# Optimization experiments

Hardware: AMD Instinct MI355X
Metric: run time of the kernel (lower is better)

The kernel has to match this reference:

```python
import jax, jax.numpy as jnp
import numpy as np

N = 50000          # site nodes
L = 32             # max URL token length
E = 64             # embed_size
H = 128            # hidden_size
E_SIM = 800000     # edges per relation in blocks
E_SUB = 200000     # 'sim' edges classified at the end
NEG = 0.01         # LeakyReLU negative slope

def leaky(x):
    return jnp.where(x >= 0, x, NEG * x)

def lstm_final(x, mask, Wih, Whh, b, reverse):
    # x: [N, L, E], mask: [N, L] bool. Returns packed-sequence final hidden [N, E].
    if reverse:
        x = x[:, ::-1, :]
        mask = mask[:, ::-1]
    h0 = jnp.zeros((x.shape[0], Whh.shape[1]), x.dtype)
    def step(carry, inp):
        h, c = carry
        xt, mt = inp
        g = xt @ Wih.T + h @ Whh.T + b
        i, f, gg, o = jnp.split(g, 4, axis=-1)  # PyTorch gate order i,f,g,o
        cn = jax.nn.sigmoid(f) * c + jax.nn.sigmoid(i) * jnp.tanh(gg)
        hn = jax.nn.sigmoid(o) * jnp.tanh(cn)
        m = mt[:, None]
        return (jnp.where(m, hn, h), jnp.where(m, cn, c)), None
    (h, _), _ = jax.lax.scan(step, (h0, h0), (x.transpose(1, 0, 2), mask.T))
    return h

def graph_conv(h, src, dst, W, b):
    # DGL GraphConv, norm='both': D_dst^{-1/2} A D_src^{-1/2} h W + b  (degrees clamped to >=1)
    n = h.shape[0]
    ones = jnp.ones(src.shape[0], h.dtype)
    out_deg = jnp.clip(jax.ops.segment_sum(ones, src, num_segments=n), 1.0)
    in_deg = jnp.clip(jax.ops.segment_sum(ones, dst, num_segments=n), 1.0)
    feat = h * jax.lax.rsqrt(out_deg)[:, None]
    if W.shape[0] > W.shape[1]:
        feat = feat @ W  # project before gather/scatter when in_dim > out_dim (as DGL does)
        rst = jax.ops.segment_sum(feat[src], dst, num_segments=n)
    else:
        rst = jax.ops.segment_sum(feat[src], dst, num_segments=n) @ W
    return rst * jax.lax.rsqrt(in_deg)[:, None] + b

def setup_inputs():
    key = jax.random.key(0)
    ks = iter(jax.random.split(key, 64))
    def nrm(shape, scale=0.05):
        return jax.random.normal(next(ks), shape, dtype=jnp.float32) * scale
    inp = {}
    inp["inputs_s"] = jax.random.randint(next(ks), (N, L), 0, 128)
    lengths = jax.random.randint(next(ks), (N,), 1, L + 1)
    inp["inputs_sm"] = (jnp.arange(L)[None, :] < lengths[:, None]).astype(jnp.int32)
    inp["inputs_c"] = jax.random.randint(next(ks), (N, 1), 0, 101)
    inp["inputs_co"] = jax.random.randint(next(ks), (N, 1), 0, 92)
    inp["inputs_sl"] = jax.random.randint(next(ks), (N, 1), 0, 6)
    for name, m in [("sim_src", E_SIM), ("sim_dst", E_SIM), ("user_src", E_SIM),
                    ("user_dst", E_SIM), ("esub_src", E_SUB), ("esub_dst", E_SUB)]:
        inp[name] = jax.random.randint(next(ks), (m,), 0, N)
    inp["emb_url"] = nrm((128, E)); inp["emb_cat"] = nrm((101, E))
    inp["emb_country"] = nrm((92, E)); inp["emb_sl"] = nrm((6, E))
    for d in ("f", "b"):
        inp["Wih_" + d] = nrm((4 * E, E)); inp["Whh_" + d] = nrm((4 * E, E))
        inp["b_" + d] = nrm((4 * E,))  # b_ih + b_hh folded into one bias
    inp["fc_W"] = nrm((E, 2 * E)); inp["fc_b"] = nrm((E,))
    for i, din in enumerate([4 * E, H]):
        for rel in ("sim", "user"):
            inp["gcn%d_%s_W" % (i, rel)] = nrm((din, H))
            inp["gcn%d_%s_b" % (i, rel)] = nrm((H,))
    inp["cls_W1"] = nrm((H, 2 * H)); inp["cls_b1"] = nrm((H,))
    inp["bn_g"] = jnp.ones((H,), jnp.float32); inp["bn_b"] = jnp.zeros((H,), jnp.float32)
    inp["cls_W2"] = nrm((2, H)); inp["cls_b2"] = nrm((2,))
    return inp

def reference(inputs_s, inputs_sm, inputs_c, inputs_co, inputs_sl,
              sim_src, sim_dst, user_src, user_dst, esub_src, esub_dst,
              emb_url, emb_cat, emb_country, emb_sl,
              Wih_f, Whh_f, b_f, Wih_b, Whh_b, b_b, fc_W, fc_b,
              gcn0_sim_W, gcn0_sim_b, gcn0_user_W, gcn0_user_b,
              gcn1_sim_W, gcn1_sim_b, gcn1_user_W, gcn1_user_b,
              cls_W1, cls_b1, bn_g, bn_b, cls_W2, cls_b2):
    mask = inputs_sm.astype(bool)
    x = emb_url[inputs_s]                                # [N, L, E]
    hf = lstm_final(x, mask, Wih_f, Whh_f, b_f, False)   # h_n[0]
    hb = lstm_final(x, mask, Wih_b, Whh_b, b_b, True)    # h_n[1]
    h_url = leaky(jnp.concatenate([hf, hb], -1) @ fc_W.T + fc_b)  # dropout = identity (eval)
    h = jnp.concatenate([h_url, emb_cat[inputs_c[:, 0]],
                         emb_country[inputs_co[:, 0]], emb_sl[inputs_sl[:, 0]]], -1)  # [N, 4E]
    layers = [(gcn0_sim_W, gcn0_sim_b, gcn0_user_W, gcn0_user_b),
              (gcn1_sim_W, gcn1_sim_b, gcn1_user_W, gcn1_user_b)]
    for Ws, bs, Wu, bu in layers:  # HeteroGraphConv aggregate='sum'
        h = leaky(graph_conv(h, sim_src, sim_dst, Ws, bs)
                  + graph_conv(h, user_src, user_dst, Wu, bu))
    feat = jnp.concatenate([h[esub_src], h[esub_dst]], -1)  # [E_SUB, 2H]
    z = feat @ cls_W1.T + cls_b1
    z = (z - z.mean(0)) * jax.lax.rsqrt(z.var(0) + 1e-5) * bn_g + bn_b  # BatchNorm1d (batch stats)
    z = jnp.maximum(z, 0.0)
    return z @ cls_W2.T + cls_b2
```

## Files before the change

kernel.cpp:

```cpp
#include <hip/hip_runtime.h>
#include <hip/hip_bf16.h>
#include <stdint.h>

#define N_NODES 50000
#define SEQ_L   32
#define NE_BIG  800000
#define NE_SUB  200000
#define DSTRIDE 64
#define BNREP   64

typedef __hip_bfloat16 bf16;
typedef unsigned short u16;
typedef unsigned int u32;
typedef _Float16 f16;
typedef _Float16 v8h __attribute__((ext_vector_type(8)));
typedef float v4f __attribute__((ext_vector_type(4)));

#if __has_builtin(__builtin_amdgcn_exp2f)
#define EXP2(x) __builtin_amdgcn_exp2f(x)
#else
extern "C" __device__ float __ocml_native_exp2_f32(float);
#define EXP2(x) __ocml_native_exp2_f32(x)
#endif
#define LOG2E  1.4426950408889634f
#define LOG2E2 2.8853900817779268f
#define GCLAMP 43.280851226668902f

__device__ __forceinline__ float b2f(bf16 x) { return __bfloat162float(x); }
__device__ __forceinline__ float leakyf(float v) { return v >= 0.f ? v : 0.01f * v; }
__device__ __forceinline__ u16 f2h_bits(float x) { f16 h = (f16)x; u16 b; __builtin_memcpy(&b, &h, 2); return b; }
__device__ __forceinline__ float h2f(u16 b) { f16 h; __builtin_memcpy(&h, &b, 2); return (float)h; }
__device__ __forceinline__ uint pack2h(float a, float b) { return (uint)f2h_bits(a) | ((uint)f2h_bits(b) << 16); }

__device__ __forceinline__ float ldf(const void* p, int i, int isbf) {
  return isbf ? b2f(((const bf16*)p)[i]) : ((const float*)p)[i];
}

__device__ __forceinline__ int detect_isbf(const u16* __restrict__ u) {
  __shared__ int insane;
  if (threadIdx.x == 0) insane = 0;
  __syncthreads();
  int expo = (u[threadIdx.x * 2] >> 7) & 0xFF;
  if (expo >= 147) atomicAdd(&insane, 1);
  __syncthreads();
  return insane == 0;
}

#define NBUCK   391
#define BSHIFT  7
#define BCAP    3072
#define P1_EPT   32
#define P1_CHUNK (256 * P1_EPT)
#define P1_NCH   ((NE_BIG + P1_CHUNK - 1) / P1_CHUNK)
#define P1_BLOCKS (P1_NCH * 2)

struct PrepArgs {
  const void* Whh_f; const void* Whh_b; const void* fc_W; const void* cls_W1;
  const void* g0sW; const void* g0uW; const void* g1sW; const void* g1uW;
  const void* emb_cat; const void* emb_country; const void* emb_sl;
  const void* fc_b; const void* cls_b1; const void* g0sb; const void* g0ub;
  const void* g1sb; const void* g1ub; const void* bn_g; const void* bn_b;
  const void* cls_W2; const void* cls_b2;
  const void* emb_url; const void* Wih_f; const void* b_f; const void* Wih_b; const void* b_b;
  f16* Whh_h; u16* Bfc; u16* BW1; u16* Bg0; u16* Bg1;
  u16* embc_h; u16* embco_h; u16* embs_h;
  float* fcb; float* b1; float* g0sbP; float* g0ubP; float* g1sbP; float* g1ubP;
  float* bngP; float* bnbP; float* W2P; float* b2P;
  int* dflag;
  float* Xperm;
  const int* sm; int* lens; int* cnt33;
  const int* s0; const int* d0; const int* s1; const int* d1;
  int* cnt4; int* gcur; u32* bucket;
};

__global__ __launch_bounds__(256) void prep_graph_kernel(PrepArgs A) {
  const int bid = blockIdx.x;
  const int t = threadIdx.x;

  __shared__ u32 stage[P1_CHUNK];
  __shared__ int hcnt[NBUCK];
  __shared__ int hstart[NBUCK];
  __shared__ int gbase[NBUCK];
  __shared__ int scanbuf[512];

  if (bid < P1_BLOCKS) {
    const int rel = bid & 1;
    const int chunk = bid >> 1;
    const int* s = rel ? A.s1 : A.s0;
    const int* d = rel ? A.d1 : A.d0;
    int* outdeg = A.cnt4 + (size_t)rel * 2 * N_NODES;
    int* gcur = A.gcur + rel * NBUCK;
    u32* bbuf = A.bucket + (size_t)rel * NBUCK * BCAP;
    const int e0 = chunk * P1_CHUNK;
    const int cn = min(NE_BIG - e0, P1_CHUNK);

    for (int b = t; b < NBUCK; b += 256) hcnt[b] = 0;
    __syncthreads();
#pragma unroll
    for (int k = 0; k < P1_EPT; ++k) {
      int i = t + k * 256;
      if (i < cn) {
        int sv = s[e0 + i], dv = d[e0 + i];
        atomicAdd(&outdeg[sv], 1);
        atomicAdd(&hcnt[dv >> BSHIFT], 1);
      }
    }
    __syncthreads();
    scanbuf[t] = (t < NBUCK) ? hcnt[t] : 0;
    scanbuf[t + 256] = (t + 256 < NBUCK) ? hcnt[t + 256] : 0;
    __syncthreads();
    for (int off = 1; off < 512; off <<= 1) {
      int a0 = (t >= off) ? scanbuf[t - off] : 0;
      int a1 = (t + 256 >= off) ? scanbuf[t + 256 - off] : 0;
      __syncthreads();
      scanbuf[t] += a0;
      scanbuf[t + 256] += a1;
      __syncthreads();
    }
    for (int b = t; b < NBUCK; b += 256) {
      int c = hcnt[b];
      int st = scanbuf[b] - c;
      hstart[b] = st;
      gbase[b] = (c > 0) ? atomicAdd(&gcur[b], c) : 0;
      scanbuf[b] = st;
    }
    __syncthreads();
#pragma unroll
    for (int k = 0; k < P1_EPT; ++k) {
      int i = t + k * 256;
      if (i < cn) {
        int sv = s[e0 + i], dv = d[e0 + i];
        int b = dv >> BSHIFT;
        int pos = atomicAdd(&scanbuf[b], 1);
        stage[pos] = ((u32)b << 23) | ((u32)sv << 7) | (u32)(dv & 127);
      }
    }
    __syncthreads();
    for (int i = t; i < cn; i += 256) {
      u32 r = stage[i];
      int b = r >> 23;
      int o = gbase[b] + (i - hstart[b]);
      if (o < BCAP) bbuf[(size_t)b * BCAP + o] = r;
    }
    return;
  }

  const int b = bid - P1_BLOCKS;

  if (b >= 990) {
    int i = (b - 990) * 256 + t;
    if (i >= N_NODES) return;
    int len = 0;
#pragma unroll
    for (int tt = 0; tt < SEQ_L; ++tt) len += __builtin_nontemporal_load(A.sm + i * SEQ_L + tt);
    A.lens[i] = len;
    atomicAdd(&A.cnt33[len], 1);
    return;
  }

  const int isbf = detect_isbf((const u16*)A.emb_url);
  auto cpy = [&](const void* s, float* d, int n, int boff) {
    int i = (b - boff) * 256 + t;
    if (i < n) d[i] = ldf(s, i, isbf);
  };
  auto cvh = [&](const void* s, u16* d, int n, int boff) {
    int i = (b - boff) * 256 + t;
    if (i < n) d[i] = f2h_bits(ldf(s, i, isbf));
  };
  auto cvhW = [&](const void* s, u16* d, int boff) {
    int i = (b - boff) * 256 + t;
    float sc = ((i >> 12) == 2) ? LOG2E2 : LOG2E;
    d[i] = f2h_bits(ldf(s, i, isbf) * sc);
  };
  auto trh = [&](const void* s, u16* d, int R, int C, int KOFF, int boff) {
    int i = (b - boff) * 256 + t;
    if (i < R * C) { int r = i / C, c = i % C; d[c * 256 + KOFF + r] = f2h_bits(ldf(s, i, isbf)); }
  };
  if      (b <   64) cvhW(A.Whh_f, (u16*)A.Whh_h, 0);
  else if (b <  128) cvhW(A.Whh_b, (u16*)(A.Whh_h + 16384), 64);
  else if (b <  160) cvh(A.fc_W, A.Bfc, 8192, 128);
  else if (b <  288) cvh(A.cls_W1, A.BW1, 32768, 160);
  else if (b <  416) trh(A.g0sW, A.Bg0, 256, 128, 0, 288);
  else if (b <  544) trh(A.g0uW, A.Bg0 + 128 * 256, 256, 128, 0, 416);
  else if (b <  608) trh(A.g1sW, A.Bg1, 128, 128, 0, 544);
  else if (b <  672) trh(A.g1uW, A.Bg1, 128, 128, 128, 608);
  else if (b <  698) cvh(A.emb_cat, A.embc_h, 6464, 672);
  else if (b <  721) cvh(A.emb_country, A.embco_h, 5888, 698);
  else if (b <  723) cvh(A.emb_sl, A.embs_h, 384, 721);
  else if (b <  724) cpy(A.fc_b, A.fcb, 64, 723);
  else if (b <  725) cpy(A.cls_b1, A.b1, 128, 724);
  else if (b <  726) cpy(A.g0sb, A.g0sbP, 128, 725);
  else if (b <  727) cpy(A.g0ub, A.g0ubP, 128, 726);
  else if (b <  728) cpy(A.g1sb, A.g1sbP, 128, 727);
  else if (b <  729) cpy(A.g1ub, A.g1ubP, 128, 728);
  else if (b <  730) cpy(A.bn_g, A.bngP, 128, 729);
  else if (b <  731) cpy(A.bn_b, A.bnbP, 128, 730);
  else if (b <  732) cpy(A.cls_W2, A.W2P, 256, 731);
  else if (b <  733) { cpy(A.cls_b2, A.b2P, 2, 732); if (t == 0) A.dflag[0] = isbf; }
  else if (b <  989) {
    int bb = b - 733;
    int dir = bb >> 7;
    int v = bb & 127;
    const void* Wih = dir ? A.Wih_b : A.Wih_f;
    const void* bias = dir ? A.b_b : A.b_f;
    __shared__ float embL[64];
    if (t < 64) embL[t] = ldf(A.emb_url, v * 64 + t, isbf);
    __syncthreads();
    float acc = ldf(bias, t, isbf);
#pragma unroll 8
    for (int j = 0; j < 64; ++j) acc += embL[j] * ldf(Wih, t * 64 + j, isbf);
    int g = t >> 6, unit = t & 63;
    float sc = (g == 2) ? LOG2E2 : LOG2E;
    A.Xperm[(size_t)dir * 128 * 256 + v * 256 + unit * 4 + g] = acc * sc;
  }
}
#define PG_BLOCKS (P1_BLOCKS + 1186)

__global__ __launch_bounds__(256) void permfill_rsq_kernel(
    const int* __restrict__ lens, const int* __restrict__ cnt33, int* __restrict__ cur33,
    int* __restrict__ perm,
    int* __restrict__ cnt4, float* __restrict__ rsq4,
    const u32* __restrict__ bucket, const int* __restrict__ gcur,
    u16* __restrict__ col0, u16* __restrict__ col1)
{
  const int b = blockIdx.x, t = threadIdx.x;
  __shared__ u16 colL[128 * DSTRIDE];
  __shared__ int curL[128];

  if (b < 196) {
    int i = b * 256 + t;
    if (i >= N_NODES) return;
    int len = lens[i];
    int base = 0;
    for (int l = len + 1; l <= SEQ_L; ++l) base += cnt33[l];
    int p = atomicAdd(&cur33[len], 1);
    perm[base + p] = i;
  } else if (b < 196 + 2 * NBUCK) {
    int k = b - 196;
    int rel = k / NBUCK;
    int bk = k % NBUCK;
    const u32* bb = bucket + ((size_t)rel * NBUCK + bk) * BCAP;
    u16* col = rel ? col1 : col0;
    int cnt = gcur[rel * NBUCK + bk];
    if (cnt > BCAP) cnt = BCAP;
    if (t < 128) curL[t] = 0;
    __syncthreads();
    for (int i = t; i < cnt; i += 256) {
      u32 r = bb[i];
      int dl = r & 127;
      int sv = (r >> 7) & 0xFFFF;
      int p = atomicAdd(&curL[dl], 1);
      if (p < DSTRIDE) colL[dl * DSTRIDE + p] = (u16)sv;
    }
    __syncthreads();
    const int node0 = bk << BSHIFT;
    for (int idx = t; idx < 128 * (DSTRIDE / 2); idx += 256) {
      int row = idx >> 5;
      int node = node0 + row;
      if (node < N_NODES)
        ((uint*)(col + (size_t)node * DSTRIDE))[idx & 31] = ((const uint*)colL)[idx];
    }
    if (t < 128) {
      int node = node0 + t;
      if (node < N_NODES) {
        int c = curL[t];
        cnt4[rel * 2 * N_NODES + N_NODES + node] = c;
        float cc = (c < 1) ? 1.f : (float)c;
        rsq4[rel * 2 * N_NODES + N_NODES + node] = __builtin_amdgcn_rsqf(cc);
      }
    }
  } else {
    int idx = (b - 196 - 2 * NBUCK) * 256 + t;
    int i;
    if (idx < N_NODES) i = idx;
    else if (idx < 2 * N_NODES) i = idx + N_NODES;
    else return;
    int c = cnt4[i]; if (c < 1) c = 1;
    rsq4[i] = __builtin_amdgcn_rsqf((float)c);
  }
}
#define PR_BLOCKS (196 + 2 * NBUCK + 391)

__global__ __launch_bounds__(256, 4) void lstm_mfma_kernel(
    const int* __restrict__ perm, const int* __restrict__ lens,
    const int* __restrict__ toksg,
    const float* __restrict__ Xperm,
    const f16* __restrict__ Whh_h,
    u16* __restrict__ hcat_h,
    int nnodes)
{
  __shared__ __align__(16) f16 H[2][64 * 72];
  __shared__ int permL[64];
  __shared__ int lensL[64];
  __shared__ int cutL[SEQ_L + 1];
  const int tid = threadIdx.x;
  const int w = tid >> 6;
  const int lane = tid & 63;
  const int quad = lane >> 4;
  const int lid = lane & 15;
  const int dir = blockIdx.y;
  char* Hc = (char*)&H[0][0];

  if (tid < 64) {
    int gid = blockIdx.x * 64 + tid;
    int node = -1, len = 0;
    if (gid < nnodes) { node = perm[gid]; len = lens[node]; }
    permL[tid] = node; lensL[tid] = len;
  }
  {
    uint* Hz = (uint*)Hc;
    for (int i = tid; i < 2 * 64 * 72 / 2; i += 256) Hz[i] = 0u;
  }
  __syncthreads();
  if (tid <= SEQ_L) {
    int c = 0;
#pragma unroll 8
    for (int n = 0; n < 64; ++n) c += (lensL[n] > tid) ? 1 : 0;
    cutL[tid] = c;
  }
  for (int idx = tid; idx < 64 * SEQ_L; idx += 256) {
    int node = idx >> 5, tp = idx & 31;
    int len = lensL[node];
    if (tp < len) {
      int s = dir ? (len - 1 - tp) : tp;
      int i = s * 64 + node;
      Hc[(i >> 4) * 144 + 128 + (i & 15)] = (char)toksg[(size_t)permL[node] * SEQ_L + tp];
    }
  }
  __syncthreads();
  const int tmax = lensL[0];

  const f16* Wd = Whh_h + (size_t)dir * 256 * 64;
  v8h Bf[4][2];
#pragma unroll
  for (int g = 0; g < 4; ++g)
#pragma unroll
    for (int kf = 0; kf < 2; ++kf)
      Bf[g][kf] = *(const v8h*)(Wd + (g * 64 + w * 16 + lid) * 64 + kf * 32 + quad * 8);

  float creg[16];
  f16 hreg[16];
#pragma unroll
  for (int i = 0; i < 16; ++i) { creg[i] = 0.f; hreg[i] = (f16)0.f; }

  const char* Xp = (const char*)(Xperm + (size_t)dir * 128 * 256);
  const uint xlane = (uint)((w * 16 + lid) * 16);

  for (int step = 0; step < tmax; ++step) {
    const int rb = step & 1, wb = rb ^ 1;
    const int cut = cutL[step];
#pragma unroll
    for (int mt = 0; mt < 4; ++mt) {
      uint tok4 = *(const uint*)(Hc + (step * 4 + mt) * 144 + 128 + quad * 4);
      float4 xr[4];
#pragma unroll
      for (int r = 0; r < 4; ++r) {
        uint tok = (tok4 >> (8 * r)) & 255u;
        xr[r] = *(const float4*)(Xp + (tok << 10) + xlane);
      }
      const f16* hb = &H[rb][0];
      int arow = (mt * 16 + lid) * 72 + quad * 8;
      v8h a0 = *(const v8h*)(hb + arow);
      v8h a1 = *(const v8h*)(hb + arow + 32);
      v4f acc[4];
      acc[0] = (v4f){xr[0].x, xr[1].x, xr[2].x, xr[3].x};
      acc[1] = (v4f){xr[0].y, xr[1].y, xr[2].y, xr[3].y};
      acc[2] = (v4f){xr[0].z, xr[1].z, xr[2].z, xr[3].z};
      acc[3] = (v4f){xr[0].w, xr[1].w, xr[2].w, xr[3].w};
#pragma unroll
      for (int g = 0; g < 4; ++g) {
        acc[g] = __builtin_amdgcn_mfma_f32_16x16x32_f16(a0, Bf[g][0], acc[g], 0, 0, 0);
        acc[g] = __builtin_amdgcn_mfma_f32_16x16x32_f16(a1, Bf[g][1], acc[g], 0, 0, 0);
      }
#pragma unroll
      for (int r = 0; r < 4; ++r) {
        int idx = mt * 4 + r;
        int nd = mt * 16 + quad * 4 + r;
        bool act = nd < cut;
        float gi = acc[0][r];
        float gf = acc[1][r];
        float gG = acc[2][r];
        float go = acc[3][r];
        float A = EXP2(-gi);
        float B = EXP2(-gf);
        float C = EXP2(-go);
        float D = EXP2(fminf(gG, GCLAMP));
        float sf = __builtin_amdgcn_rcpf(1.f + B);
        float sitg = (D - 1.f) * __builtin_amdgcn_rcpf((1.f + A) * (D + 1.f));
        float cn = sf * creg[idx] + sitg;
        float E = EXP2(fminf(cn * LOG2E2, GCLAMP));
        float hn = (E - 1.f) * __builtin_amdgcn_rcpf((1.f + C) * (E + 1.f));
        if (act) { creg[idx] = cn; hreg[idx] = (f16)hn; }
        H[wb][nd * 72 + w * 16 + lid] = hreg[idx];
      }
    }
    __syncthreads();
  }
#pragma unroll
  for (int mt = 0; mt < 4; ++mt)
#pragma unroll
    for (int r = 0; r < 4; ++r) {
      int nd = mt * 16 + quad * 4 + r;
      int gnode = permL[nd];
      if (gnode >= 0) {
        u16 bits; f16 hv = hreg[mt * 4 + r]; __builtin_memcpy(&bits, &hv, 2);
        hcat_h[(size_t)gnode * 128 + dir * 64 + w * 16 + lid] = bits;
      }
    }
}

template<int K, int COLS, int AMODE, bool LEAKY, int OHS, bool EMB, bool BNS>
__global__ __launch_bounds__(256) void mfma_gemm(
    const u16* __restrict__ Ah,
    const int* __restrict__ esrc, const int* __restrict__ edst, const u16* __restrict__ Fh,
    const u16* __restrict__ B,
    const float* __restrict__ bias, const float* __restrict__ bias2,
    const float* __restrict__ rs0, const float* __restrict__ rs1,
    u16* __restrict__ outh0, u16* __restrict__ outh1,
    const int* __restrict__ ic, const int* __restrict__ ico, const int* __restrict__ isl,
    const u16* __restrict__ ech, const u16* __restrict__ ecoh, const u16* __restrict__ eslh,
    float* __restrict__ bnsums,
    int nrows)
{
  constexpr int AST = K + 8;
  constexpr int ABYTES = 64 * AST * 2;
  constexpr int EBYTES = 64 * 129 * 4;
  constexpr int SBYTES = (ABYTES > EBYTES) ? ABYTES : EBYTES;
  __shared__ __align__(16) char smem[SBYTES];
  u16* As = (u16*)smem;
  float* Es = (float*)smem;
  __shared__ int idxL[128];
  __shared__ float bnred[BNS ? 512 : 1];

  const int tid = threadIdx.x;
  const int w = tid >> 6;
  const int lane = tid & 63;
  const int quad = lane >> 4;
  const int lid = lane & 15;
  const int r0 = blockIdx.x * 64;

  if (AMODE == 2) {
    if (tid < 64) {
      int row = r0 + tid;
      idxL[tid] = (row < nrows) ? esrc[row] : -1;
      idxL[64 + tid] = (row < nrows) ? edst[row] : -1;
    }
    __syncthreads();
    for (int idx = tid; idx < 64 * (K / 8); idx += 256) {
      int rn = idx / (K / 8), seg = idx % (K / 8);
      int half = seg >> 4, k8 = seg & 15;
      int base = idxL[half * 64 + rn];
      uint4 v = {0u, 0u, 0u, 0u};
      if (base >= 0) v = *(const uint4*)(Fh + (size_t)base * 128 + k8 * 8);
      *(uint4*)(As + rn * AST + seg * 8) = v;
    }
  } else {
    for (int idx = tid; idx < 64 * (K / 8); idx += 256) {
      int rn = idx / (K / 8), c8 = idx % (K / 8);
      int row = r0 + rn;
      uint4 v = {0u, 0u, 0u, 0u};
      if (row < nrows) v = *(const uint4*)(Ah + (size_t)row * K + c8 * 8);
      *(uint4*)(As + rn * AST + c8 * 8) = v;
    }
  }
  __syncthreads();

  constexpr int NT = COLS / 16;
  v4f acc[NT];
#pragma unroll
  for (int i = 0; i < NT; ++i) acc[i] = (v4f){0.f, 0.f, 0.f, 0.f};

  for (int kb = 0; kb < K / 32; ++kb) {
    v8h a = *(const v8h*)((const f16*)As + (w * 16 + lid) * AST + kb * 32 + quad * 8);
#pragma unroll
    for (int ct = 0; ct < NT; ++ct) {
      v8h b = *(const v8h*)((const f16*)B + (size_t)(ct * 16 + lid) * K + kb * 32 + quad * 8);
      acc[ct] = __builtin_amdgcn_mfma_f32_16x16x32_f16(a, b, acc[ct], 0, 0, 0);
    }
  }

  constexpr int NH = (COLS > 128) ? 2 : 1;
  constexpr int CH = COLS / NH;
  float bs = 0.f, bs2 = 0.f;
#pragma unroll
  for (int h = 0; h < NH; ++h) {
    __syncthreads();
#pragma unroll
    for (int ct = 0; ct < CH / 16; ++ct) {
      int ctg = h * (CH / 16) + ct;
#pragma unroll
      for (int r = 0; r < 4; ++r)
        Es[(w * 16 + quad * 4 + r) * 129 + ct * 16 + lid] = acc[ctg][r];
    }
    __syncthreads();
    for (int idx = tid; idx < 64 * CH; idx += 256) {
      int rn = idx / CH, c = idx % CH;
      int row = r0 + rn;
      float v = 0.f;
      if (row < nrows) {
        v = Es[rn * 129 + c];
        if (bias) v += bias[h * CH + c];
        if (bias2) v += bias2[h * CH + c];
        if (LEAKY) v = leakyf(v);
        const float* rs = (h == 0) ? rs0 : rs1;
        if (rs) v *= rs[row];
        u16* oh = (h == 0) ? outh0 : outh1;
        oh[(size_t)row * OHS + c] = f2h_bits(v);
      }
      if (BNS) { bs += v; bs2 += v * v; }
    }
  }
  if (BNS) {
    bnred[tid] = bs;
    bnred[256 + tid] = bs2;
    __syncthreads();
    if (tid < 128) {
      float* bnp = bnsums + (size_t)(blockIdx.x & (BNREP - 1)) * 256;
      atomicAdd(&bnp[tid], bnred[tid] + bnred[tid + 128]);
      atomicAdd(&bnp[128 + tid], bnred[256 + tid] + bnred[384 + tid]);
    }
  }
  if (EMB) {
    for (int idx = tid; idx < 64 * 192; idx += 256) {
      int rn = idx / 192, j = idx % 192;
      int row = r0 + rn;
      if (row >= nrows) continue;
      u16 v;
      if (j < 64)       v = ech [ic [row] * 64 + j];
      else if (j < 128) v = ecoh[ico[row] * 64 + (j - 64)];
      else              v = eslh[isl[row] * 64 + (j - 128)];
      outh0[(size_t)row * OHS + 64 + j] = v;
    }
  }
}

__global__ __launch_bounds__(256) void gather_merge0_kernel(
    const u16* __restrict__ colS, const int* __restrict__ cntS, const u16* __restrict__ Ps,
    const u16* __restrict__ colU, const int* __restrict__ cntU, const u16* __restrict__ Pu,
    const float* __restrict__ rsS, const float* __restrict__ rsU,
    const float* __restrict__ bS, const float* __restrict__ bU,
    u16* __restrict__ outh, int nnodes)
{
  int wave = threadIdx.x >> 6;
  int lane = threadIdx.x & 63;
  int node = __builtin_amdgcn_readfirstlane(blockIdx.x * 4 + wave);
  if (node >= nnodes) return;
  const uint* PS2 = (const uint*)Ps;
  const uint* PU2 = (const uint*)Pu;
  float2 aS = make_float2(0.f, 0.f), aU = make_float2(0.f, 0.f);
  {
    const u16* col = colS + (size_t)node * DSTRIDE;
    int cnt = min(cntS[node], DSTRIDE);
    int e = 0;
    for (; e + 4 <= cnt; e += 4) {
      uint v0 = PS2[(size_t)col[e] * 64 + lane];
      uint v1 = PS2[(size_t)col[e + 1] * 64 + lane];
      uint v2 = PS2[(size_t)col[e + 2] * 64 + lane];
      uint v3 = PS2[(size_t)col[e + 3] * 64 + lane];
      aS.x += h2f((u16)v0) + h2f((u16)v1) + h2f((u16)v2) + h2f((u16)v3);
      aS.y += h2f((u16)(v0 >> 16)) + h2f((u16)(v1 >> 16)) + h2f((u16)(v2 >> 16)) + h2f((u16)(v3 >> 16));
    }
    for (; e < cnt; ++e) {
      uint v = PS2[(size_t)col[e] * 64 + lane];
      aS.x += h2f((u16)v); aS.y += h2f((u16)(v >> 16));
    }
  }
  {
    const u16* col = colU + (size_t)node * DSTRIDE;
    int cnt = min(cntU[node], DSTRIDE);
    int e = 0;
    for (; e + 4 <= cnt; e += 4) {
      uint v0 = PU2[(size_t)col[e] * 64 + lane];
      uint v1 = PU2[(size_t)col[e + 1] * 64 + lane];
      uint v2 = PU2[(size_t)col[e + 2] * 64 + lane];
      uint v3 = PU2[(size_t)col[e + 3] * 64 + lane];
      aU.x += h2f((u16)v0) + h2f((u16)v1) + h2f((u16)v2) + h2f((u16)v3);
      aU.y += h2f((u16)(v0 >> 16)) + h2f((u16)(v1 >> 16)) + h2f((u16)(v2 >> 16)) + h2f((u16)(v3 >> 16));
    }
    for (; e < cnt; ++e) {
      uint v = PU2[(size_t)col[e] * 64 + lane];
      aU.x += h2f((u16)v); aU.y += h2f((u16)(v >> 16));
    }
  }
  float rS = rsS[node], rU = rsU[node];
  float2 bsv = ((const float2*)bS)[lane];
  float2 buv = ((const float2*)bU)[lane];
  float o0 = leakyf(aS.x * rS + bsv.x + aU.x * rU + buv.x);
  float o1 = leakyf(aS.y * rS + bsv.y + aU.y * rU + buv.y);
  ((uint*)outh)[(size_t)node * 64 + lane] = pack2h(o0, o1);
}

__global__ __launch_bounds__(256) void gather_cat1_kernel(
    const u16* __restrict__ colS, const int* __restrict__ cntS,
    const u16* __restrict__ colU, const int* __restrict__ cntU,
    const u16* __restrict__ Fh,
    const float* __restrict__ rsoutS, const float* __restrict__ rsoutU,
    const float* __restrict__ rsinS, const float* __restrict__ rsinU,
    u16* __restrict__ Acat, int nnodes)
{
  int wave = threadIdx.x >> 6;
  int lane = threadIdx.x & 63;
  int node = __builtin_amdgcn_readfirstlane(blockIdx.x * 4 + wave);
  if (node >= nnodes) return;
  const uint* F2 = (const uint*)Fh;
  float2 aS = make_float2(0.f, 0.f), aU = make_float2(0.f, 0.f);
  {
    const u16* col = colS + (size_t)node * DSTRIDE;
    int cnt = min(cntS[node], DSTRIDE);
    int e = 0;
    for (; e + 2 <= cnt; e += 2) {
      int s0 = col[e], s1 = col[e + 1];
      float c0 = rsoutS[s0], c1 = rsoutS[s1];
      uint v0 = F2[(size_t)s0 * 64 + lane];
      uint v1 = F2[(size_t)s1 * 64 + lane];
      aS.x += c0 * h2f((u16)v0) + c1 * h2f((u16)v1);
      aS.y += c0 * h2f((u16)(v0 >> 16)) + c1 * h2f((u16)(v1 >> 16));
    }
    for (; e < cnt; ++e) {
      int s = col[e]; float c = rsoutS[s];
      uint v = F2[(size_t)s * 64 + lane];
      aS.x += c * h2f((u16)v); aS.y += c * h2f((u16)(v >> 16));
    }
  }
  {
    const u16* col = colU + (size_t)node * DSTRIDE;
    int cnt = min(cntU[node], DSTRIDE);
    int e = 0;
    for (; e + 2 <= cnt; e += 2) {
      int s0 = col[e], s1 = col[e + 1];
      float c0 = rsoutU[s0], c1 = rsoutU[s1];
      uint v0 = F2[(size_t)s0 * 64 + lane];
      uint v1 = F2[(size_t)s1 * 64 + lane];
      aU.x += c0 * h2f((u16)v0) + c1 * h2f((u16)v1);
      aU.y += c0 * h2f((u16)(v0 >> 16)) + c1 * h2f((u16)(v1 >> 16));
    }
    for (; e < cnt; ++e) {
      int s = col[e]; float c = rsoutU[s];
      uint v = F2[(size_t)s * 64 + lane];
      aU.x += c * h2f((u16)v); aU.y += c * h2f((u16)(v >> 16));
    }
  }
  float rs = rsinS[node], ru = rsinU[node];
  ((uint*)Acat)[(size_t)node * 128 + lane] = pack2h(aS.x * rs, aS.y * rs);
  ((uint*)Acat)[(size_t)node * 128 + 64 + lane] = pack2h(aU.x * ru, aU.y * ru);
}

__global__ __launch_bounds__(256) void out_kernel(
    const u16* __restrict__ zh, const float* __restrict__ bnsums,
    const float* __restrict__ g, const float* __restrict__ bb, float M,
    const float* __restrict__ W2, const float* __restrict__ b2,
    void* __restrict__ out, int Mi, const int* __restrict__ flag)
{
  __shared__ float lds[128 * 65];
  __shared__ float red[64 * 8];
  __shared__ float ssL[256];
  const int tid = threadIdx.x;
  const int n = tid & 63;
  const int q = __builtin_amdgcn_readfirstlane(tid >> 6);
  const int r0 = blockIdx.x * 64;
  if (tid < 128) {
    float s = 0.f, s2 = 0.f;
#pragma unroll 8
    for (int r = 0; r < BNREP; ++r) {
      s  += bnsums[r * 256 + tid];
      s2 += bnsums[r * 256 + 128 + tid];
    }
    float mean = s / M;
    float var = s2 / M - mean * mean;
    float sc = g[tid] * __builtin_amdgcn_rsqf(var + 1e-5f);
    ssL[tid] = sc;
    ssL[128 + tid] = bb[tid] - mean * sc;
  }
  for (int idx = tid; idx < 64 * 128; idx += 256) {
    int rn = idx >> 7, j = idx & 127;
    int row = r0 + rn;
    lds[j * 65 + rn] = (row < Mi) ? h2f(zh[(size_t)row * 128 + j]) : 0.f;
  }
  __syncthreads();
  float a0 = 0.f, a1 = 0.f;
#pragma unroll 8
  for (int jj = 0; jj < 32; ++jj) {
    int j = q * 32 + jj;
    float y = lds[j * 65 + n] * ssL[j] + ssL[128 + j];
    y = y > 0.f ? y : 0.f;
    a0 += y * W2[j];
    a1 += y * W2[128 + j];
  }
  red[n * 8 + q * 2 + 0] = a0;
  red[n * 8 + q * 2 + 1] = a1;
  __syncthreads();
  if (q == 0 && (r0 + n) < Mi) {
    float o0 = red[n * 8] + red[n * 8 + 2] + red[n * 8 + 4] + red[n * 8 + 6] + b2[0];
    float o1 = red[n * 8 + 1] + red[n * 8 + 3] + red[n * 8 + 5] + red[n * 8 + 7] + b2[1];
    size_t oi = (size_t)(r0 + n) * 2;
    if (*flag) {
      ((bf16*)out)[oi + 0] = __float2bfloat16(o0);
      ((bf16*)out)[oi + 1] = __float2bfloat16(o1);
    } else {
      ((float*)out)[oi + 0] = o0;
      ((float*)out)[oi + 1] = o1;
    }
  }
}

extern "C" void kernel_launch(void* const* d_in, const int* in_sizes, int n_in,
                              void* d_out, int out_size, void* d_ws, size_t ws_size,
                              hipStream_t stream) {
  (void)in_sizes; (void)n_in; (void)out_size; (void)ws_size;
  const int N = N_NODES;
  const int* inputs_s  = (const int*)d_in[0];
  const int* inputs_sm = (const int*)d_in[1];
  const int* inputs_c  = (const int*)d_in[2];
  const int* inputs_co = (const int*)d_in[3];
  const int* inputs_sl = (const int*)d_in[4];
  const int* sim_src   = (const int*)d_in[5];
  const int* sim_dst   = (const int*)d_in[6];
  const int* user_src  = (const int*)d_in[7];
  const int* user_dst  = (const int*)d_in[8];
  const int* esub_src  = (const int*)d_in[9];
  const int* esub_dst  = (const int*)d_in[10];

  char* base = (char*)d_ws;
  size_t off = 0;
  auto alloc = [&](size_t bytes) -> char* {
    char* p = base + off;
    off += (bytes + 255) & ~(size_t)255;
    return p;
  };
  int* dflag    = (int*)alloc(256);
  f16* Whh_h    = (f16*)alloc(2 * 256 * 64 * 2);
  float* Xperm  = (float*)alloc(2 * 128 * 256 * 4);
  u16* Bfc      = (u16*)alloc(64 * 128 * 2);
  u16* BW1      = (u16*)alloc(128 * 256 * 2);
  u16* Bg0      = (u16*)alloc(256 * 256 * 2);
  u16* Bg1      = (u16*)alloc(128 * 256 * 2);
  u16* P_embc_h = (u16*)alloc(6464 * 2);
  u16* P_embco_h= (u16*)alloc(5888 * 2);
  u16* P_embs_h = (u16*)alloc(384 * 2);
  float* P_fcb  = (float*)alloc(64 * 4);
  float* P_b1   = (float*)alloc(128 * 4);
  float* P_g0sb = (float*)alloc(128 * 4);
  float* P_g0ub = (float*)alloc(128 * 4);
  float* P_g1sb = (float*)alloc(128 * 4);
  float* P_g1ub = (float*)alloc(128 * 4);
  float* P_bng  = (float*)alloc(128 * 4);
  float* P_bnb  = (float*)alloc(128 * 4);
  float* P_W2   = (float*)alloc(256 * 4);
  float* P_b2   = (float*)alloc(2 * 4);
  int* lens     = (int*)alloc((size_t)N * 4);
  int* perm     = (int*)alloc((size_t)N * 4);
  float* rsq4   = (float*)alloc((size_t)4 * N * 4);
  char* zbase   = alloc((size_t)4 * N * 4 + 4096 + BNREP * 256 * 4);
  int* cnt4     = (int*)zbase;
  int* cnt33    = (int*)(zbase + (size_t)4 * N * 4);
  int* cur33    = cnt33 + 64;
  int* gcur     = (int*)(zbase + (size_t)4 * N * 4 + 512);
  float* bnsums = (float*)(zbase + (size_t)4 * N * 4 + 4096);
  const size_t zbytes = (size_t)4 * N * 4 + 4096 + BNREP * 256 * 4;
  char* bufA = alloc((size_t)N * 256 * 4);
  char* bufB = alloc((size_t)N * 256 * 2);
  char* bufC = alloc((size_t)N * 256 * 2);
  char* bufE = alloc((size_t)N * 128 * 2);
  u16* h_h     = (u16*)bufA;
  u16* zh      = (u16*)bufA;
  u16* col_sim = (u16*)(bufA + (size_t)N * 256 * 2);
  u16* col_usr = (u16*)(bufA + (size_t)N * 256 * 2 + (size_t)N * DSTRIDE * 2);
  u16* hcat_h = (u16*)bufB;
  u16* h1_h   = (u16*)bufB;
  u32* bucket = (u32*)bufC;
  u16* Ps_h   = (u16*)bufC;
  u16* Pu_h   = Ps_h + (size_t)N * 128;
  u16* Acat   = (u16*)bufC;
  u16* F_h    = (u16*)bufE;

  const int NB64 = (N + 63) / 64;
  const int NBZ  = (NE_SUB + 63) / 64;

  hipMemsetAsync(zbase, 0, zbytes, stream);

  PrepArgs PA;
  PA.Whh_f = d_in[16]; PA.Whh_b = d_in[19]; PA.fc_W = d_in[21]; PA.cls_W1 = d_in[31];
  PA.g0sW = d_in[23]; PA.g0uW = d_in[25]; PA.g1sW = d_in[27]; PA.g1uW = d_in[29];
  PA.emb_cat = d_in[12]; PA.emb_country = d_in[13]; PA.emb_sl = d_in[14];
  PA.fc_b = d_in[22]; PA.cls_b1 = d_in[32]; PA.g0sb = d_in[24]; PA.g0ub = d_in[26];
  PA.g1sb = d_in[28]; PA.g1ub = d_in[30]; PA.bn_g = d_in[33]; PA.bn_b = d_in[34];
  PA.cls_W2 = d_in[35]; PA.cls_b2 = d_in[36];
  PA.emb_url = d_in[11]; PA.Wih_f = d_in[15]; PA.b_f = d_in[17]; PA.Wih_b = d_in[18]; PA.b_b = d_in[20];
  PA.Whh_h = Whh_h; PA.Bfc = Bfc; PA.BW1 = BW1; PA.Bg0 = Bg0; PA.Bg1 = Bg1;
  PA.embc_h = P_embc_h; PA.embco_h = P_embco_h; PA.embs_h = P_embs_h;
  PA.fcb = P_fcb; PA.b1 = P_b1; PA.g0sbP = P_g0sb; PA.g0ubP = P_g0ub; PA.g1sbP = P_g1sb; PA.g1ubP = P_g1ub;
  PA.bngP = P_bng; PA.bnbP = P_bnb; PA.W2P = P_W2; PA.b2P = P_b2;
  PA.dflag = dflag; PA.Xperm = Xperm;
  PA.sm = inputs_sm; PA.lens = lens; PA.cnt33 = cnt33;
  PA.s0 = sim_src; PA.d0 = sim_dst; PA.s1 = user_src; PA.d1 = user_dst;
  PA.cnt4 = cnt4; PA.gcur = gcur; PA.bucket = bucket;
  prep_graph_kernel<<<PG_BLOCKS, 256, 0, stream>>>(PA);

  permfill_rsq_kernel<<<PR_BLOCKS, 256, 0, stream>>>(lens, cnt33, cur33, perm, cnt4, rsq4,
                                                     bucket, gcur, col_sim, col_usr);

  lstm_mfma_kernel<<<dim3(NB64, 2), 256, 0, stream>>>(perm, lens, inputs_s, Xperm, Whh_h, hcat_h, N);

  mfma_gemm<128, 64, 1, true, 256, true, false><<<NB64, 256, 0, stream>>>(
      hcat_h, nullptr, nullptr, nullptr, Bfc, P_fcb, nullptr, nullptr, nullptr,
      h_h, nullptr, inputs_c, inputs_co, inputs_sl, P_embc_h, P_embco_h, P_embs_h, nullptr, N);

  mfma_gemm<256, 256, 1, false, 128, false, false><<<NB64, 256, 0, stream>>>(
      h_h, nullptr, nullptr, nullptr, Bg0, nullptr, nullptr, rsq4, rsq4 + 2 * N,
      Ps_h, Pu_h, nullptr, nullptr, nullptr, nullptr, nullptr, nullptr, nullptr, N);

  gather_merge0_kernel<<<(N + 3) / 4, 256, 0, stream>>>(col_sim, cnt4 + N, Ps_h,
                                                        col_usr, cnt4 + 3 * N, Pu_h,
                                                        rsq4 + N, rsq4 + 3 * N, P_g0sb, P_g0ub, h1_h, N);

  gather_cat1_kernel<<<(N + 3) / 4, 256, 0, stream>>>(col_sim, cnt4 + N, col_usr, cnt4 + 3 * N, h1_h,
                                                      rsq4, rsq4 + 2 * N, rsq4 + N, rsq4 + 3 * N, Acat, N);

  mfma_gemm<256, 128, 1, true, 128, false, false><<<NB64, 256, 0, stream>>>(
      Acat, nullptr, nullptr, nullptr, Bg1, P_g1sb, P_g1ub, nullptr, nullptr,
      F_h, nullptr, nullptr, nullptr, nullptr, nullptr, nullptr, nullptr, nullptr, N);

  mfma_gemm<256, 128, 2, false, 128, false, true><<<NBZ, 256, 0, stream>>>(
      nullptr, esub_src, esub_dst, F_h, BW1, P_b1, nullptr, nullptr, nullptr,
      zh, nullptr, nullptr, nullptr, nullptr, nullptr, nullptr, nullptr, bnsums, NE_SUB);

  out_kernel<<<NBZ, 256, 0, stream>>>(zh, bnsums, P_bng, P_bnb, (float)NE_SUB,
                                      P_W2, P_b2, d_out, NE_SUB, dflag);
}
```

Measured before the change: 1.060 ms.

## Project node features through classifier W1 before edge gather; overlap CSR build with LSTM

The classifier's first linear layer is split by linearity into a source half and a destination half. Both halves are applied per node (50k rows) with one GEMM, and a light edge kernel then gathers and adds the two projections plus bias while accumulating BatchNorm statistics. This replaces the per-edge gather-GEMM over 200k edges. Separately, the CSR column building and degree rsqrt work moves out of a standalone kernel into extra blocks of the LSTM launch, so it can overlap with the recurrent work; this adds some grid complexity and reuses LSTM shared memory.

```diff
diff --git a/kernel.cpp b/kernel.cpp
--- a/kernel.cpp
+++ b/kernel.cpp
@@ -53,6 +53,8 @@
 #define P1_CHUNK (256 * P1_EPT)
 #define P1_NCH   ((NE_BIG + P1_CHUNK - 1) / P1_CHUNK)
 #define P1_BLOCKS (P1_NCH * 2)
+#define LSTM_XB  782
+#define LSTM_EXTRA 587
 
 struct PrepArgs {
   const void* Whh_f; const void* Whh_b; const void* fc_W; const void* cls_W1;
@@ -179,7 +181,11 @@
   if      (b <   64) cvhW(A.Whh_f, (u16*)A.Whh_h, 0);
   else if (b <  128) cvhW(A.Whh_b, (u16*)(A.Whh_h + 16384), 64);
   else if (b <  160) cvh(A.fc_W, A.Bfc, 8192, 128);
-  else if (b <  288) cvh(A.cls_W1, A.BW1, 32768, 160);
+  else if (b <  288) {
+    int i = (b - 160) * 256 + t;
+    int j = i >> 8, k = i & 255;
+    A.BW1[(size_t)(((k >> 7) * 128 + j) * 128 + (k & 127))] = f2h_bits(ldf(A.cls_W1, i, isbf));
+  }
   else if (b <  416) trh(A.g0sW, A.Bg0, 256, 128, 0, 288);
   else if (b <  544) trh(A.g0uW, A.Bg0 + 128 * 256, 256, 128, 0, 416);
   else if (b <  608) trh(A.g1sW, A.Bg1, 128, 128, 0, 544);
@@ -216,70 +222,19 @@
 }
 #define PG_BLOCKS (P1_BLOCKS + 1186)
 
-__global__ __launch_bounds__(256) void permfill_rsq_kernel(
+__global__ __launch_bounds__(256) void permfill_kernel(
     const int* __restrict__ lens, const int* __restrict__ cnt33, int* __restrict__ cur33,
-    int* __restrict__ perm,
-    int* __restrict__ cnt4, float* __restrict__ rsq4,
-    const u32* __restrict__ bucket, const int* __restrict__ gcur,
-    u16* __restrict__ col0, u16* __restrict__ col1)
+    int* __restrict__ perm)
 {
-  const int b = blockIdx.x, t = threadIdx.x;
-  __shared__ u16 colL[128 * DSTRIDE];
-  __shared__ int curL[128];
-
-  if (b < 196) {
-    int i = b * 256 + t;
-    if (i >= N_NODES) return;
-    int len = lens[i];
-    int base = 0;
-    for (int l = len + 1; l <= SEQ_L; ++l) base += cnt33[l];
-    int p = atomicAdd(&cur33[len], 1);
-    perm[base + p] = i;
-  } else if (b < 196 + 2 * NBUCK) {
-    int k = b - 196;
-    int rel = k / NBUCK;
-    int bk = k % NBUCK;
-    const u32* bb = bucket + ((size_t)rel * NBUCK + bk) * BCAP;
-    u16* col = rel ? col1 : col0;
-    int cnt = gcur[rel * NBUCK + bk];
-    if (cnt > BCAP) cnt = BCAP;
-    if (t < 128) curL[t] = 0;
-    __syncthreads();
-    for (int i = t; i < cnt; i += 256) {
-      u32 r = bb[i];
-      int dl = r & 127;
-      int sv = (r >> 7) & 0xFFFF;
-      int p = atomicAdd(&curL[dl], 1);
-      if (p < DSTRIDE) colL[dl * DSTRIDE + p] = (u16)sv;
-    }
-    __syncthreads();
-    const int node0 = bk << BSHIFT;
-    for (int idx = t; idx < 128 * (DSTRIDE / 2); idx += 256) {
-      int row = idx >> 5;
-      int node = node0 + row;
-      if (node < N_NODES)
-        ((uint*)(col + (size_t)node * DSTRIDE))[idx & 31] = ((const uint*)colL)[idx];
-    }
-    if (t < 128) {
-      int node = node0 + t;
-      if (node < N_NODES) {
-        int c = curL[t];
-        cnt4[rel * 2 * N_NODES + N_NODES + node] = c;
-        float cc = (c < 1) ? 1.f : (float)c;
-        rsq4[rel * 2 * N_NODES + N_NODES + node] = __builtin_amdgcn_rsqf(cc);
-      }
-    }
-  } else {
-    int idx = (b - 196 - 2 * NBUCK) * 256 + t;
-    int i;
-    if (idx < N_NODES) i = idx;
-    else if (idx < 2 * N_NODES) i = idx + N_NODES;
-    else return;
-    int c = cnt4[i]; if (c < 1) c = 1;
-    rsq4[i] = __builtin_amdgcn_rsqf((float)c);
-  }
-}
-#define PR_BLOCKS (196 + 2 * NBUCK + 391)
+  int i = blockIdx.x * 256 + threadIdx.x;
+  if (i >= N_NODES) return;
+  int len = lens[i];
+  int base = 0;
+  for (int l = len + 1; l <= SEQ_L; ++l) base += cnt33[l];
+  int p = atomicAdd(&cur33[len], 1);
+  perm[base + p] = i;
+}
+#define PF_BLOCKS 196
 
 __global__ __launch_bounds__(256, 4) void lstm_mfma_kernel(
     const int* __restrict__ perm, const int* __restrict__ lens,
@@ -287,6 +242,9 @@
     const float* __restrict__ Xperm,
     const f16* __restrict__ Whh_h,
     u16* __restrict__ hcat_h,
+    const u32* __restrict__ bucket, const int* __restrict__ gcur,
+    u16* __restrict__ col0, u16* __restrict__ col1,
+    int* __restrict__ cnt4, float* __restrict__ rsq4,
     int nnodes)
 {
   __shared__ __align__(16) f16 H[2][64 * 72];
@@ -294,15 +252,66 @@
   __shared__ int lensL[64];
   __shared__ int cutL[SEQ_L + 1];
   const int tid = threadIdx.x;
+  const int bx = blockIdx.x;
+  const int dir = blockIdx.y;
+  char* Hc = (char*)&H[0][0];
+
+  if (bx >= LSTM_XB) {
+    int e = (bx - LSTM_XB) + dir * LSTM_EXTRA;
+    u16* colL = (u16*)Hc;
+    int* curL = (int*)(Hc + 16384);
+    if (e < 2 * NBUCK) {
+      int rel = e / NBUCK;
+      int bk = e % NBUCK;
+      const u32* bb = bucket + ((size_t)rel * NBUCK + bk) * BCAP;
+      u16* col = rel ? col1 : col0;
+      int cnt = gcur[rel * NBUCK + bk];
+      if (cnt > BCAP) cnt = BCAP;
+      if (tid < 128) curL[tid] = 0;
+      __syncthreads();
+      for (int i = tid; i < cnt; i += 256) {
+        u32 r = bb[i];
+        int dl = r & 127;
+        int sv = (r >> 7) & 0xFFFF;
+        int p = atomicAdd(&curL[dl], 1);
+        if (p < DSTRIDE) colL[dl * DSTRIDE + p] = (u16)sv;
+      }
+      __syncthreads();
+      const int node0 = bk << BSHIFT;
+      for (int idx = tid; idx < 128 * (DSTRIDE / 2); idx += 256) {
+        int row = idx >> 5;
+        int node = node0 + row;
+        if (node < N_NODES)
+          ((uint*)(col + (size_t)node * DSTRIDE))[idx & 31] = ((const uint*)colL)[idx];
+      }
+      if (tid < 128) {
+        int node = node0 + tid;
+        if (node < N_NODES) {
+          int c = curL[tid];
+          cnt4[rel * 2 * N_NODES + N_NODES + node] = c;
+          float cc = (c < 1) ? 1.f : (float)c;
+          rsq4[rel * 2 * N_NODES + N_NODES + node] = __builtin_amdgcn_rsqf(cc);
+        }
+      }
+    } else if (e < 2 * NBUCK + 391) {
+      int idx = (e - 2 * NBUCK) * 256 + tid;
+      int i;
+      if (idx < N_NODES) i = idx;
+      else if (idx < 2 * N_NODES) i = idx + N_NODES;
+      else return;
+      int c = cnt4[i]; if (c < 1) c = 1;
+      rsq4[i] = __builtin_amdgcn_rsqf((float)c);
+    }
+    return;
+  }
+
   const int w = tid >> 6;
   const int lane = tid & 63;
   const int quad = lane >> 4;
   const int lid = lane & 15;
-  const int dir = blockIdx.y;
-  char* Hc = (char*)&H[0][0];
 
   if (tid < 64) {
-    int gid = blockIdx.x * 64 + tid;
+    int gid = bx * 64 + tid;
     int node = -1, len = 0;
     if (gid < nnodes) { node = perm[gid]; len = lens[node]; }
     permL[tid] = node; lensL[tid] = len;
@@ -409,17 +418,15 @@
     }
 }
 
-template<int K, int COLS, int AMODE, bool LEAKY, int OHS, bool EMB, bool BNS>
+template<int K, int COLS, bool LEAKY, int OHS, bool EMB>
 __global__ __launch_bounds__(256) void mfma_gemm(
     const u16* __restrict__ Ah,
-    const int* __restrict__ esrc, const int* __restrict__ edst, const u16* __restrict__ Fh,
     const u16* __restrict__ B,
     const float* __restrict__ bias, const float* __restrict__ bias2,
     const float* __restrict__ rs0, const float* __restrict__ rs1,
     u16* __restrict__ outh0, u16* __restrict__ outh1,
     const int* __restrict__ ic, const int* __restrict__ ico, const int* __restrict__ isl,
     const u16* __restrict__ ech, const u16* __restrict__ ecoh, const u16* __restrict__ eslh,
-    float* __restrict__ bnsums,
     int nrows)
 {
   constexpr int AST = K + 8;
@@ -429,8 +436,6 @@
   __shared__ __align__(16) char smem[SBYTES];
   u16* As = (u16*)smem;
   float* Es = (float*)smem;
-  __shared__ int idxL[128];
-  __shared__ float bnred[BNS ? 512 : 1];
 
   const int tid = threadIdx.x;
   const int w = tid >> 6;
@@ -439,29 +444,12 @@
   const int lid = lane & 15;
   const int r0 = blockIdx.x * 64;
 
-  if (AMODE == 2) {
-    if (tid < 64) {
-      int row = r0 + tid;
-      idxL[tid] = (row < nrows) ? esrc[row] : -1;
-      idxL[64 + tid] = (row < nrows) ? edst[row] : -1;
-    }
-    __syncthreads();
-    for (int idx = tid; idx < 64 * (K / 8); idx += 256) {
-      int rn = idx / (K / 8), seg = idx % (K / 8);
-      int half = seg >> 4, k8 = seg & 15;
-      int base = idxL[half * 64 + rn];
-      uint4 v = {0u, 0u, 0u, 0u};
-      if (base >= 0) v = *(const uint4*)(Fh + (size_t)base * 128 + k8 * 8);
-      *(uint4*)(As + rn * AST + seg * 8) = v;
-    }
-  } else {
-    for (int idx = tid; idx < 64 * (K / 8); idx += 256) {
-      int rn = idx / (K / 8), c8 = idx % (K / 8);
-      int row = r0 + rn;
-      uint4 v = {0u, 0u, 0u, 0u};
-      if (row < nrows) v = *(const uint4*)(Ah + (size_t)row * K + c8 * 8);
-      *(uint4*)(As + rn * AST + c8 * 8) = v;
-    }
+  for (int idx = tid; idx < 64 * (K / 8); idx += 256) {
+    int rn = idx / (K / 8), c8 = idx % (K / 8);
+    int row = r0 + rn;
+    uint4 v = {0u, 0u, 0u, 0u};
+    if (row < nrows) v = *(const uint4*)(Ah + (size_t)row * K + c8 * 8);
+    *(uint4*)(As + rn * AST + c8 * 8) = v;
   }
   __syncthreads();
 
@@ -481,7 +469,6 @@
 
   constexpr int NH = (COLS > 128) ? 2 : 1;
   constexpr int CH = COLS / NH;
-  float bs = 0.f, bs2 = 0.f;
 #pragma unroll
   for (int h = 0; h < NH; ++h) {
     __syncthreads();
@@ -496,9 +483,8 @@
     for (int idx = tid; idx < 64 * CH; idx += 256) {
       int rn = idx / CH, c = idx % CH;
       int row = r0 + rn;
-      float v = 0.f;
       if (row < nrows) {
-        v = Es[rn * 129 + c];
+        float v = Es[rn * 129 + c];
         if (bias) v += bias[h * CH + c];
         if (bias2) v += bias2[h * CH + c];
         if (LEAKY) v = leakyf(v);
@@ -507,17 +493,6 @@
         u16* oh = (h == 0) ? outh0 : outh1;
         oh[(size_t)row * OHS + c] = f2h_bits(v);
       }
-      if (BNS) { bs += v; bs2 += v * v; }
-    }
-  }
-  if (BNS) {
-    bnred[tid] = bs;
-    bnred[256 + tid] = bs2;
-    __syncthreads();
-    if (tid < 128) {
-      float* bnp = bnsums + (size_t)(blockIdx.x & (BNREP - 1)) * 256;
-      atomicAdd(&bnp[tid], bnred[tid] + bnred[tid + 128]);
-      atomicAdd(&bnp[128 + tid], bnred[256 + tid] + bnred[384 + tid]);
     }
   }
   if (EMB) {
@@ -531,6 +506,48 @@
       else              v = eslh[isl[row] * 64 + (j - 128)];
       outh0[(size_t)row * OHS + 64 + j] = v;
     }
+  }
+}
+
+__global__ __launch_bounds__(256) void edge_cls_kernel(
+    const int* __restrict__ esrc, const int* __restrict__ edst,
+    const u16* __restrict__ G12,
+    const float* __restrict__ b1,
+    u16* __restrict__ zh, float* __restrict__ bnsums, int ne)
+{
+  __shared__ float redS[512];
+  __shared__ float redQ[512];
+  const int tid = threadIdx.x;
+  const int w = tid >> 6;
+  const int lane = tid & 63;
+  const uint* Gu = (const uint*)G12;
+  float2 bsv = ((const float2*)b1)[lane];
+  float s0 = 0.f, s1 = 0.f, q0 = 0.f, q1 = 0.f;
+  const int e0 = blockIdx.x * 64 + w * 16;
+#pragma unroll
+  for (int k = 0; k < 16; ++k) {
+    int e = e0 + k;
+    if (e < ne) {
+      int sv = esrc[e], dv = edst[e];
+      uint a = Gu[(size_t)sv * 128 + lane];
+      uint b = Gu[(size_t)dv * 128 + 64 + lane];
+      float z0 = h2f((u16)a) + h2f((u16)b) + bsv.x;
+      float z1 = h2f((u16)(a >> 16)) + h2f((u16)(b >> 16)) + bsv.y;
+      ((uint*)zh)[(size_t)e * 64 + lane] = pack2h(z0, z1);
+      s0 += z0; s1 += z1; q0 += z0 * z0; q1 += z1 * z1;
+    }
+  }
+  redS[w * 128 + lane * 2 + 0] = s0;
+  redS[w * 128 + lane * 2 + 1] = s1;
+  redQ[w * 128 + lane * 2 + 0] = q0;
+  redQ[w * 128 + lane * 2 + 1] = q1;
+  __syncthreads();
+  if (tid < 128) {
+    float s = redS[tid] + redS[128 + tid] + redS[256 + tid] + redS[384 + tid];
+    float q = redQ[tid] + redQ[128 + tid] + redQ[256 + tid] + redQ[384 + tid];
+    float* bnp = bnsums + (size_t)(blockIdx.x & (BNREP - 1)) * 256;
+    atomicAdd(&bnp[tid], s);
+    atomicAdd(&bnp[128 + tid], q);
   }
 }
 
@@ -731,7 +748,7 @@
   f16* Whh_h    = (f16*)alloc(2 * 256 * 64 * 2);
   float* Xperm  = (float*)alloc(2 * 128 * 256 * 4);
   u16* Bfc      = (u16*)alloc(64 * 128 * 2);
-  u16* BW1      = (u16*)alloc(128 * 256 * 2);
+  u16* BW1      = (u16*)alloc(256 * 128 * 2);
   u16* Bg0      = (u16*)alloc(256 * 256 * 2);
   u16* Bg1      = (u16*)alloc(128 * 256 * 2);
   u16* P_embc_h = (u16*)alloc(6464 * 2);
@@ -771,6 +788,7 @@
   u16* Ps_h   = (u16*)bufC;
   u16* Pu_h   = Ps_h + (size_t)N * 128;
   u16* Acat   = (u16*)bufC;
+  u16* G12    = (u16*)bufC;
   u16* F_h    = (u16*)bufE;
 
   const int NB64 = (N + 63) / 64;
@@ -796,18 +814,19 @@
   PA.cnt4 = cnt4; PA.gcur = gcur; PA.bucket = bucket;
   prep_graph_kernel<<<PG_BLOCKS, 256, 0, stream>>>(PA);
 
-  permfill_rsq_kernel<<<PR_BLOCKS, 256, 0, stream>>>(lens, cnt33, cur33, perm, cnt4, rsq4,
-                                                     bucket, gcur, col_sim, col_usr);
-
-  lstm_mfma_kernel<<<dim3(NB64, 2), 256, 0, stream>>>(perm, lens, inputs_s, Xperm, Whh_h, hcat_h, N);
-
-  mfma_gemm<128, 64, 1, true, 256, true, false><<<NB64, 256, 0, stream>>>(
-      hcat_h, nullptr, nullptr, nullptr, Bfc, P_fcb, nullptr, nullptr, nullptr,
-      h_h, nullptr, inputs_c, inputs_co, inputs_sl, P_embc_h, P_embco_h, P_embs_h, nullptr, N);
-
-  mfma_gemm<256, 256, 1, false, 128, false, false><<<NB64, 256, 0, stream>>>(
-      h_h, nullptr, nullptr, nullptr, Bg0, nullptr, nullptr, rsq4, rsq4 + 2 * N,
-      Ps_h, Pu_h, nullptr, nullptr, nullptr, nullptr, nullptr, nullptr, nullptr, N);
+  permfill_kernel<<<PF_BLOCKS, 256, 0, stream>>>(lens, cnt33, cur33, perm);
+
+  lstm_mfma_kernel<<<dim3(LSTM_XB + LSTM_EXTRA, 2), 256, 0, stream>>>(
+      perm, lens, inputs_s, Xperm, Whh_h, hcat_h,
+      bucket, gcur, col_sim, col_usr, cnt4, rsq4, N);
+
+  mfma_gemm<128, 64, true, 256, true><<<NB64, 256, 0, stream>>>(
+      hcat_h, Bfc, P_fcb, nullptr, nullptr, nullptr,
+      h_h, nullptr, inputs_c, inputs_co, inputs_sl, P_embc_h, P_embco_h, P_embs_h, N);
+
+  mfma_gemm<256, 256, false, 128, false><<<NB64, 256, 0, stream>>>(
+      h_h, Bg0, nullptr, nullptr, rsq4, rsq4 + 2 * N,
+      Ps_h, Pu_h, nullptr, nullptr, nullptr, nullptr, nullptr, nullptr, N);
 
   gather_merge0_kernel<<<(N + 3) / 4, 256, 0, stream>>>(col_sim, cnt4 + N, Ps_h,
                                                         col_usr, cnt4 + 3 * N, Pu_h,
@@ -816,13 +835,15 @@
   gather_cat1_kernel<<<(N + 3) / 4, 256, 0, stream>>>(col_sim, cnt4 + N, col_usr, cnt4 + 3 * N, h1_h,
                                                       rsq4, rsq4 + 2 * N, rsq4 + N, rsq4 + 3 * N, Acat, N);
 
-  mfma_gemm<256, 128, 1, true, 128, false, false><<<NB64, 256, 0, stream>>>(
-      Acat, nullptr, nullptr, nullptr, Bg1, P_g1sb, P_g1ub, nullptr, nullptr,
-      F_h, nullptr, nullptr, nullptr, nullptr, nullptr, nullptr, nullptr, nullptr, N);
-
-  mfma_gemm<256, 128, 2, false, 128, false, true><<<NBZ, 256, 0, stream>>>(
-      nullptr, esub_src, esub_dst, F_h, BW1, P_b1, nullptr, nullptr, nullptr,
-      zh, nullptr, nullptr, nullptr, nullptr, nullptr, nullptr, nullptr, bnsums, NE_SUB);
+  mfma_gemm<256, 128, true, 128, false><<<NB64, 256, 0, stream>>>(
+      Acat, Bg1, P_g1sb, P_g1ub, nullptr, nullptr,
+      F_h, nullptr, nullptr, nullptr, nullptr, nullptr, nullptr, nullptr, N);
+
+  mfma_gemm<128, 256, false, 256, false><<<NB64, 256, 0, stream>>>(
+      F_h, BW1, nullptr, nullptr, nullptr, nullptr,
+      G12, G12 + 128, nullptr, nullptr, nullptr, nullptr, nullptr, nullptr, N);
+
+  edge_cls_kernel<<<NBZ, 256, 0, stream>>>(esub_src, esub_dst, G12, P_b1, zh, bnsums, NE_SUB);
 
   out_kernel<<<NBZ, 256, 0, stream>>>(zh, bnsums, P_bng, P_bnb, (float)NE_SUB,
                                       P_W2, P_b2, d_out, NE_SUB, dflag);
```

Measured after the change: 1.002 ms. 5.5% less time.
